# Kernel optimization log

Hardware: AMD Instinct MI355X
Metric: run time of the kernel (lower is better)

Reference implementation:

```python
import jax, jax.numpy as jnp
import numpy as np
import math

D_MODEL = 1024
MEM_SIZE = 4096
N_HEADS = 8
BATCH = 4
SEQ = 1024
TOP_K = min(SEQ, MEM_SIZE // 10)  # 409, matches torch: min(seq_len, memory_size//10)
UPDATE_RATE = 0.01


def _gelu(x):
    return jax.nn.gelu(x, approximate=False)  # torch nn.GELU default (erf)


def setup_inputs() -> dict:
    key = jax.random.key(0)
    ks = jax.random.split(key, 26)
    w = lambda k, shape, s=0.02: (jax.random.normal(k, shape, jnp.float32) * s)
    inp = {
        "x": jax.random.normal(ks[0], (BATCH, SEQ, D_MODEL), jnp.float32),
        "memory_bank": jax.random.normal(ks[1], (MEM_SIZE, D_MODEL), jnp.float32) * 0.1,
        "memory_indices": jax.random.randint(ks[2], (BATCH, TOP_K), 0, MEM_SIZE, jnp.int32),
        # memory_encoder: Linear -> GELU -> Linear
        "enc_w1": w(ks[3], (D_MODEL, D_MODEL)), "enc_b1": jnp.zeros((D_MODEL,), jnp.float32),
        "enc_w2": w(ks[4], (D_MODEL, D_MODEL)), "enc_b2": jnp.zeros((D_MODEL,), jnp.float32),
        # MultiheadAttention in/out projections
        "wq": w(ks[5], (D_MODEL, D_MODEL)), "bq": jnp.zeros((D_MODEL,), jnp.float32),
        "wk": w(ks[6], (D_MODEL, D_MODEL)), "bk": jnp.zeros((D_MODEL,), jnp.float32),
        "wv": w(ks[7], (D_MODEL, D_MODEL)), "bv": jnp.zeros((D_MODEL,), jnp.float32),
        "wo": w(ks[8], (D_MODEL, D_MODEL)), "bo": jnp.zeros((D_MODEL,), jnp.float32),
        # memory_decoder: Linear -> GELU -> Linear
        "dec_w1": w(ks[9], (D_MODEL, D_MODEL)), "dec_b1": jnp.zeros((D_MODEL,), jnp.float32),
        "dec_w2": w(ks[10], (D_MODEL, D_MODEL)), "dec_b2": jnp.zeros((D_MODEL,), jnp.float32),
        # LayerNorm
        "ln_g": jnp.ones((D_MODEL,), jnp.float32), "ln_b": jnp.zeros((D_MODEL,), jnp.float32),
        # importance_scorer: Linear(d,64) -> GELU -> Linear(64,1) -> Sigmoid
        "imp_w1": w(ks[11], (D_MODEL, 64)), "imp_b1": jnp.zeros((64,), jnp.float32),
        "imp_w2": w(ks[12], (64, 1)), "imp_b2": jnp.zeros((1,), jnp.float32),
    }
    return inp


def reference(x, memory_bank, memory_indices,
              enc_w1, enc_b1, enc_w2, enc_b2,
              wq, bq, wk, bk, wv, bv, wo, bo,
              dec_w1, dec_b1, dec_w2, dec_b2,
              ln_g, ln_b, imp_w1, imp_b1, imp_w2, imp_b2):
    B, L, D = x.shape
    M = memory_bank.shape[0]
    H = N_HEADS
    dh = D // H

    # memory_encoder (dropout inactive at eval)
    enc = _gelu(x @ enc_w1 + enc_b1) @ enc_w2 + enc_b2  # [B,L,D]

    # cross-attention: query = encoded input, key/value = memory bank (shared across batch)
    q = (enc @ wq + bq).reshape(B, L, H, dh)
    k = (memory_bank @ wk + bk).reshape(M, H, dh)
    v = (memory_bank @ wv + bv).reshape(M, H, dh)
    scores = jnp.einsum('blhd,mhd->bhlm', q, k) * (1.0 / math.sqrt(dh))
    attn = jax.nn.softmax(scores, axis=-1)                 # [B,H,L,M]
    ctx = jnp.einsum('bhlm,mhd->blhd', attn, v).reshape(B, L, D)
    mem_out = ctx @ wo + bo

    # memory_decoder + residual + LayerNorm
    dec = _gelu(mem_out @ dec_w1 + dec_b1) @ dec_w2 + dec_b2
    comb = x + dec
    mu = jnp.mean(comb, axis=-1, keepdims=True)
    var = jnp.var(comb, axis=-1, keepdims=True)
    out = (comb - mu) / jnp.sqrt(var + 1e-5) * ln_g + ln_b  # [B,L,D]

    # _update_memory: importance top-k select + sequential EMA scatter into memory bank
    imp = jax.nn.sigmoid(_gelu(x @ imp_w1 + imp_b1) @ imp_w2 + imp_b2)[..., 0]  # [B,L]
    _, top_idx = jax.lax.top_k(imp, TOP_K)                  # [B,K]
    top_tok = jnp.take_along_axis(x, top_idx[..., None], axis=1)  # [B,K,D]

    # faithful to the torch double loop (b outer, k inner): sequential EMA with
    # chained updates on index collisions
    flat_idx = memory_indices.reshape(-1)
    flat_tok = top_tok.reshape(-1, D)

    def body(mem, xs):
        i, t = xs
        row = (1.0 - UPDATE_RATE) * mem[i] + UPDATE_RATE * t
        return mem.at[i].set(row), None

    new_mem, _ = jax.lax.scan(body, memory_bank, (flat_idx, flat_tok))
    return out, new_mem
```

## Files before the change

### kernel.cpp

```cpp
#include <hip/hip_runtime.h>

typedef unsigned short u16;
typedef __attribute__((ext_vector_type(4))) int i4;
typedef __attribute__((ext_vector_type(4))) unsigned u4;
typedef __attribute__((ext_vector_type(4))) unsigned short us4;
typedef __attribute__((ext_vector_type(8))) short short8;
typedef __attribute__((ext_vector_type(4))) float f4;

#define D_MODEL 1024
#define ROWS 4096
#define NHEAD 8
#define DH 128
#define TOPK 409
#define NUPD 1636
#define NBATCH 4
#define MAXC 64
#define ATTNROWS 32768
#define QSCALE 0.1275174038f

__device__ __forceinline__ u16 f2bf(float f) {
  unsigned u = __builtin_bit_cast(unsigned, f);
  u += 0x7fffu + ((u >> 16) & 1u);
  return (u16)(u >> 16);
}
__device__ __forceinline__ float bf2f(u16 b) {
  unsigned u = ((unsigned)b) << 16;
  return __builtin_bit_cast(float, u);
}
__device__ __forceinline__ float ex2(float x) {
  return __builtin_amdgcn_exp2f(x);
}
__device__ __forceinline__ float gelu_f(float v) {
  return 0.5f * v * (1.0f + erff(v * 0.70710678118654752f));
}
__device__ __forceinline__ void gload16(const void* g, void* l) {
  __builtin_amdgcn_global_load_lds((const __attribute__((address_space(1))) void*)g,
                                   (__attribute__((address_space(3))) void*)l, 16, 0, 0);
}

__global__ __launch_bounds__(256) void conv2_kernel(const float* __restrict__ in0,
                                                    u16* __restrict__ out0,
                                                    const float* __restrict__ in1,
                                                    u16* __restrict__ out1, int nb) {
  int bid = blockIdx.x;
  const float* in = (bid < nb) ? in0 : in1;
  u16* out = (bid < nb) ? out0 : out1;
  int i = (bid < nb ? bid : bid - nb) * 256 + threadIdx.x;
  f4 v = ((const f4*)in)[i];
  us4 o;
  o.x = f2bf(v.x); o.y = f2bf(v.y); o.z = f2bf(v.z); o.w = f2bf(v.w);
  ((us4*)out)[i] = o;
}

__global__ __launch_bounds__(256) void wtrans8_kernel(const float* s0, const float* s1,
                                                      const float* s2, const float* s3,
                                                      const float* s4, const float* s5,
                                                      const float* s6, const float* s7,
                                                      u16* __restrict__ dst) {
  const float* srcs[8] = {s0, s1, s2, s3, s4, s5, s6, s7};
  const float* w = srcs[blockIdx.z];
  u16* wt = dst + (size_t)blockIdx.z * (1024 * 1024);
  __shared__ float t[32][33];
  int tx = threadIdx.x & 31, ty = threadIdx.x >> 5;
  int k0 = blockIdx.y * 32, n0 = blockIdx.x * 32;
  for (int r = 0; r < 4; ++r)
    t[ty + r * 8][tx] = w[(size_t)(k0 + ty + r * 8) * 1024 + n0 + tx];
  __syncthreads();
  for (int r = 0; r < 4; ++r)
    wt[(size_t)(n0 + ty + r * 8) * 1024 + k0 + tx] = f2bf(t[tx][ty + r * 8]);
}

__global__ __launch_bounds__(256) void bias_partB(const float* __restrict__ pbuf,
                                                  const float* __restrict__ bq,
                                                  const float* __restrict__ db1,
                                                  float* __restrict__ bqp,
                                                  float* __restrict__ bodp) {
  int id = blockIdx.x;
  int which = id >> 2;
  int n = (id & 3) * 256 + threadIdx.x;
  float s = 0.0f;
  for (int kb = 0; kb < 8; ++kb) s += pbuf[(size_t)(which * 8 + kb) * 1024 + n];
  float* out = which ? bodp : bqp;
  const float* badd = which ? db1 : bq;
  out[n] = s + badd[n];
}

__device__ __forceinline__ void gemm_core(const u16* __restrict__ A,
                                          const u16* __restrict__ BT,
                                          char* al, char* bl, int m0, int n0,
                                          f4 acc[4][2]) {
  const int K = 1024;
  const int tid = threadIdx.x;
  const int lane = tid & 63;
  const int g = lane >> 4, qi = lane & 15;
  const int wid = tid >> 6;
  const int wr = wid >> 1, wc = wid & 1;
  const int a0r = tid >> 2, a0b = (tid & 3) ^ ((a0r >> 1) & 3);
  const int c1 = tid + 256;
  const int a1r = c1 >> 2, a1b = (c1 & 3) ^ ((a1r >> 1) & 3);
  const int b0r = tid >> 2, b0b = (tid & 3) ^ ((b0r >> 1) & 3);

#define STAGE(buf, kt)                                                                   \
  {                                                                                      \
    const int k0_ = (kt) * 32;                                                           \
    gload16(A + (size_t)(m0 + a0r) * K + k0_ + a0b * 8, al + (buf) * 8192 + tid * 16);   \
    gload16(A + (size_t)(m0 + a1r) * K + k0_ + a1b * 8, al + (buf) * 8192 + c1 * 16);    \
    gload16(BT + (size_t)(n0 + b0r) * K + k0_ + b0b * 8, bl + (buf) * 4096 + tid * 16);  \
  }

  STAGE(0, 0);
  __syncthreads();
  int cur = 0;
  for (int kt = 0; kt < 32; ++kt) {
    if (kt + 1 < 32) STAGE(cur ^ 1, kt + 1);
    short8 af[4], bfr[2];
    for (int i = 0; i < 4; ++i) {
      int r = wr * 64 + i * 16 + qi;
      af[i] = *(const short8*)(al + cur * 8192 + r * 64 + ((g ^ ((r >> 1) & 3))) * 16);
    }
    for (int sn = 0; sn < 2; ++sn) {
      int r = wc * 32 + sn * 16 + qi;
      bfr[sn] = *(const short8*)(bl + cur * 4096 + r * 64 + ((g ^ ((r >> 1) & 3))) * 16);
    }
    for (int i = 0; i < 4; ++i)
      for (int sn = 0; sn < 2; ++sn)
        acc[i][sn] = __builtin_amdgcn_mfma_f32_16x16x32_bf16(af[i], bfr[sn], acc[i][sn], 0, 0, 0);
    __syncthreads();
    cur ^= 1;
  }
#undef STAGE
}

__global__ __launch_bounds__(256) void mega_kernel(
    const u16* __restrict__ Akv, const u16* __restrict__ BTkv,
    const float* __restrict__ bk, const float* __restrict__ bv,
    u16* __restrict__ Ck, u16* __restrict__ CvT,
    const u16* __restrict__ Ae, const u16* __restrict__ BTe,
    const float* __restrict__ be, u16* __restrict__ Ce,
    const u16* __restrict__ A0, const u16* __restrict__ B0, u16* __restrict__ C0,
    const u16* __restrict__ A1, const u16* __restrict__ B1, u16* __restrict__ C1,
    const float* __restrict__ b2, const float* __restrict__ wqf,
    const float* __restrict__ bo, const float* __restrict__ dw1,
    float* __restrict__ pbuf,
    const float* __restrict__ x, const float* __restrict__ iw1,
    const float* __restrict__ ib1, const float* __restrict__ iw2,
    const float* __restrict__ ib2, float* __restrict__ imp) {
  __shared__ __align__(16) char pool[32768];
  char* al = pool;
  char* bl = pool + 2 * 128 * 64;
  const int gid = blockIdx.x;
  const int tid = threadIdx.x;
  const int lane = tid & 63, wid = tid >> 6;
  const int g = lane >> 4, qi = lane & 15;
  const int wr = wid >> 1, wc = wid & 1;

  if (gid < 1024) {
    const int xcd = gid & 7, j = gid >> 3;
    const int m0 = ((j & 3) * 8 + xcd) * 128;
    const int n0 = (j >> 2) * 64;
    f4 acc[4][2] = {};
    gemm_core(Akv, BTkv, al, bl, m0, n0, acc);
    if (n0 < 1024) {
      for (int i = 0; i < 4; ++i) {
        int row = m0 + wr * 64 + i * 16 + g * 4;
        for (int sn = 0; sn < 2; ++sn) {
          int col = n0 + wc * 32 + sn * 16 + qi;
          float bvv = bk[col];
          for (int jj = 0; jj < 4; ++jj)
            Ck[(size_t)(row + jj) * 1024 + col] = f2bf(acc[i][sn][jj] + bvv);
        }
      }
    } else {
      u16(*t)[132] = (u16(*)[132])pool;
      __syncthreads();
      for (int i = 0; i < 4; ++i)
        for (int sn = 0; sn < 2; ++sn) {
          int nl = wc * 32 + sn * 16 + qi;
          float bvv = bv[n0 - 1024 + nl];
          for (int jj = 0; jj < 4; ++jj)
            t[nl][wr * 64 + i * 16 + g * 4 + jj] = f2bf(acc[i][sn][jj] + bvv);
        }
      __syncthreads();
      int r = tid >> 2, cg = tid & 3;
      for (int v = 0; v < 4; ++v) {
        us4 val = *(const us4*)&t[r][cg * 32 + v * 8];
        *(us4*)&CvT[(size_t)(n0 - 1024 + r) * 4096 + m0 + cg * 32 + v * 8] = val;
      }
    }
  } else if (gid < 1536) {
    const int id = gid - 1024;
    const int xcd = id & 7, j = id >> 3;
    const int m0 = ((j & 3) * 8 + xcd) * 128;
    const int n0 = (j >> 2) * 64;
    f4 acc[4][2] = {};
    gemm_core(Ae, BTe, al, bl, m0, n0, acc);
    for (int i = 0; i < 4; ++i) {
      int row = m0 + wr * 64 + i * 16 + g * 4;
      for (int sn = 0; sn < 2; ++sn) {
        int col = n0 + wc * 32 + sn * 16 + qi;
        float bv = be[col];
        for (int jj = 0; jj < 4; ++jj)
          Ce[(size_t)(row + jj) * 1024 + col] = f2bf(gelu_f(acc[i][sn][jj] + bv));
      }
    }
  } else if (gid < 1792) {
    const int id = gid - 1536;
    const int which = id >> 7, j = id & 127;
    const u16* A = which ? A1 : A0;
    const u16* BT = which ? B1 : B0;
    u16* C = which ? C1 : C0;
    const int m0 = (j >> 4) * 128, n0 = (j & 15) * 64;
    f4 acc[4][2] = {};
    gemm_core(A, BT, al, bl, m0, n0, acc);
    for (int i = 0; i < 4; ++i) {
      int row = m0 + wr * 64 + i * 16 + g * 4;
      for (int sn = 0; sn < 2; ++sn) {
        int col = n0 + wc * 32 + sn * 16 + qi;
        for (int jj = 0; jj < 4; ++jj)
          C[(size_t)(row + jj) * 1024 + col] = f2bf(acc[i][sn][jj]);
      }
    }
  } else if (gid < 1856) {
    const int lid = gid - 1792;
    const int which = lid >> 5;
    const int kb = (lid >> 2) & 7;
    const int n = (lid & 3) * 256 + tid;
    const float* bvec = which ? bo : b2;
    const float* W = which ? dw1 : wqf;
    float s = 0.0f;
    for (int k = kb * 128; k < kb * 128 + 128; ++k) s += bvec[k] * W[(size_t)k * 1024 + n];
    pbuf[(size_t)(which * 8 + kb) * 1024 + n] = s;
  } else {
    const int lid = gid - 1856;
    float* xs = (float*)pool;
    size_t base = (size_t)lid * 8192;
    for (int i = 0; i < 32; ++i) xs[tid + i * 256] = x[base + tid + i * 256];
    __syncthreads();
    int r0 = wid * 2, r1 = wid * 2 + 1;
    float a0 = 0.0f, a1 = 0.0f;
    for (int k = 0; k < 1024; ++k) {
      float wv = iw1[k * 64 + lane];
      a0 += xs[r0 * 1024 + k] * wv;
      a1 += xs[r1 * 1024 + k] * wv;
    }
    float h0 = gelu_f(a0 + ib1[lane]) * iw2[lane];
    float h1 = gelu_f(a1 + ib1[lane]) * iw2[lane];
    for (int d = 1; d < 64; d <<= 1) {
      h0 += __shfl_xor(h0, d, 64);
      h1 += __shfl_xor(h1, d, 64);
    }
    if (lane == 0) {
      imp[lid * 8 + r0] = 1.0f / (1.0f + expf(-(h0 + ib2[0])));
      imp[lid * 8 + r1] = 1.0f / (1.0f + expf(-(h1 + ib2[0])));
    }
  }
}

template <int EPI>
__global__ __launch_bounds__(256) void gemm_bt(const u16* __restrict__ A,
                                               const u16* __restrict__ BT,
                                               const float* __restrict__ bias,
                                               void* __restrict__ C) {
  __shared__ __align__(16) char al[2 * 128 * 64];
  __shared__ __align__(16) char bl[2 * 64 * 64];
  const int N = 1024;
  const int id = blockIdx.x;
  const int xcd = id & 7, j = id >> 3;
  const int m0 = ((j & 3) * 8 + xcd) * 128;
  const int n0 = (j >> 2) * 64;
  const int tid = threadIdx.x;
  const int lane = tid & 63, wid = tid >> 6;
  const int g = lane >> 4, qi = lane & 15;
  const int wr = wid >> 1, wc = wid & 1;
  f4 acc[4][2] = {};
  gemm_core(A, BT, al, bl, m0, n0, acc);
  for (int i = 0; i < 4; ++i) {
    int row = m0 + wr * 64 + i * 16 + g * 4;
    for (int sn = 0; sn < 2; ++sn) {
      int col = n0 + wc * 32 + sn * 16 + qi;
      float bv = bias[col];
      for (int jj = 0; jj < 4; ++jj) {
        float v = acc[i][sn][jj] + bv;
        if constexpr (EPI == 1) v = gelu_f(v);
        if constexpr (EPI == 4) v = v * QSCALE;
        if constexpr (EPI == 2)
          ((float*)C)[(size_t)(row + jj) * N + col] = v;
        else
          ((u16*)C)[(size_t)(row + jj) * N + col] = f2bf(v);
      }
    }
  }
}

template <int LP>
__global__ __launch_bounds__(512) void attn_kernel(const u16* __restrict__ q,
                                                   const u16* __restrict__ kp,
                                                   const u16* __restrict__ vT,
                                                   u16* __restrict__ cp0, u16* __restrict__ cp1,
                                                   u16* __restrict__ cp2, u16* __restrict__ cp3,
                                                   float* __restrict__ ml) {
  constexpr int MR = 4096 >> LP;
  constexpr int NT = MR / 64;
  __shared__ __align__(16) char kl[64 * 256];
  __shared__ __align__(16) char vl[128 * 128];
  const int id = blockIdx.x;
  const int h = id & 7;
  const int rest = id >> 3;
  const int part = rest & ((1 << LP) - 1);
  const int qblk = (rest >> LP) & 7;
  const int b = rest >> (3 + LP);
  const int tid = threadIdx.x;
  const int lane = tid & 63, wid = tid >> 6;
  const int g = lane >> 4, qi = lane & 15;
  const int qrow = b * 1024 + qblk * 128 + wid * 16 + qi;
  u16* ctp = (part == 0) ? cp0 : (part == 1) ? cp1 : (part == 2) ? cp2 : cp3;

  short8 qf[4];
  for (int kk = 0; kk < 4; ++kk)
    qf[kk] = *(const short8*)(q + (size_t)qrow * 1024 + h * 128 + kk * 32 + g * 8);

  const int kc0 = tid, kc1 = tid + 512;
  const int kr0 = kc0 >> 4, kb0 = kc0 & 15, kr1 = kc1 >> 4, kb1 = kc1 & 15;
  const int vr0 = kc0 >> 3, vb0 = kc0 & 7, vr1 = kc1 >> 3, vb1 = kc1 & 7;
  const int kd0 = kr0 * 256 + (kb0 ^ (kr0 & 7)) * 16;
  const int kd1 = kr1 * 256 + (kb1 ^ (kr1 & 7)) * 16;
  const int vd0 = vr0 * 128 + (vb0 ^ (vr0 & 7)) * 16;
  const int vd1 = vr1 * 128 + (vb1 ^ (vr1 & 7)) * 16;
  const int mbase = part * MR;
  const u16* kg0 = kp + (size_t)kr0 * 1024 + h * 128 + kb0 * 8;
  const u16* kg1 = kp + (size_t)kr1 * 1024 + h * 128 + kb1 * 8;
  const u16* vg0 = vT + (size_t)(h * 128 + vr0) * 4096 + vb0 * 8;
  const u16* vg1 = vT + (size_t)(h * 128 + vr1) * 4096 + vb1 * 8;

  i4 kreg0, kreg1, vreg0, vreg1;
#define LOADREGS(mt_)                                  \
  {                                                    \
    const int m0_ = mbase + (mt_) * 64;                \
    kreg0 = *(const i4*)(kg0 + (size_t)m0_ * 1024);    \
    kreg1 = *(const i4*)(kg1 + (size_t)m0_ * 1024);    \
    vreg0 = *(const i4*)(vg0 + m0_);                   \
    vreg1 = *(const i4*)(vg1 + m0_);                   \
  }

  f4 ct[8] = {};
  float mrun = -1e30f, lsum = 0.0f;

  LOADREGS(0);
  for (int mt = 0; mt < NT; ++mt) {
    __syncthreads();
    *(i4*)(kl + kd0) = kreg0;
    *(i4*)(kl + kd1) = kreg1;
    *(i4*)(vl + vd0) = vreg0;
    *(i4*)(vl + vd1) = vreg1;
    __syncthreads();
    if (mt + 1 < NT) LOADREGS(mt + 1);

    f4 st[4] = {};
    for (int s = 0; s < 4; ++s) {
      int n = s * 16 + qi;
      const char* krow = kl + n * 256;
      int sw = n & 7;
      for (int kk = 0; kk < 4; ++kk) {
        short8 a = *(const short8*)(krow + ((kk * 4 + g) ^ sw) * 16);
        st[s] = __builtin_amdgcn_mfma_f32_16x16x32_bf16(a, qf[kk], st[s], 0, 0, 0);
      }
    }
    float sv[16];
    float tm = -1e30f;
    for (int s = 0; s < 4; ++s)
      for (int jj = 0; jj < 4; ++jj) {
        sv[s * 4 + jj] = st[s][jj];
        tm = fmaxf(tm, st[s][jj]);
      }
    tm = fmaxf(tm, __shfl_xor(tm, 16, 64));
    tm = fmaxf(tm, __shfl_xor(tm, 32, 64));
    if (!__all(tm <= mrun + 8.0f)) {
      float mnew = fmaxf(mrun, tm);
      float r = ex2(mrun - mnew);
      lsum *= r;
      for (int i = 0; i < 8; ++i) ct[i] = ct[i] * r;
      mrun = mnew;
    }
    float psum = 0.0f;
    for (int i = 0; i < 16; ++i) {
      float p = ex2(sv[i] - mrun);
      sv[i] = p;
      psum += p;
    }
    psum += __shfl_xor(psum, 16, 64);
    psum += __shfl_xor(psum, 32, 64);
    lsum += psum;

    unsigned pk0[4], pk1[4];
    for (int s = 0; s < 4; ++s) {
      pk0[s] = (unsigned)f2bf(sv[s * 4 + 0]) | ((unsigned)f2bf(sv[s * 4 + 1]) << 16);
      pk1[s] = (unsigned)f2bf(sv[s * 4 + 2]) | ((unsigned)f2bf(sv[s * 4 + 3]) << 16);
    }
    const int src1 = qi + ((g & 1) << 5);
    const int src2 = src1 + 16;
    const bool hi = (g & 2) != 0;
    for (int p = 0; p < 2; ++p) {
      unsigned a0 = __shfl(pk0[2 * p], src1, 64), b0 = __shfl(pk0[2 * p + 1], src1, 64);
      unsigned a1 = __shfl(pk1[2 * p], src1, 64), b1 = __shfl(pk1[2 * p + 1], src1, 64);
      unsigned a2 = __shfl(pk0[2 * p], src2, 64), b2 = __shfl(pk0[2 * p + 1], src2, 64);
      unsigned a3 = __shfl(pk1[2 * p], src2, 64), b3 = __shfl(pk1[2 * p + 1], src2, 64);
      u4 bw;
      bw.x = hi ? b0 : a0; bw.y = hi ? b1 : a1; bw.z = hi ? b2 : a2; bw.w = hi ? b3 : a3;
      short8 pf = __builtin_bit_cast(short8, bw);
      for (int d = 0; d < 8; ++d) {
        int dr = d * 16 + qi;
        short8 a = *(const short8*)(vl + dr * 128 + (((p * 4 + g) ^ (dr & 7))) * 16);
        ct[d] = __builtin_amdgcn_mfma_f32_16x16x32_bf16(a, pf, ct[d], 0, 0, 0);
      }
    }
  }
#undef LOADREGS

  const int orow = ((b * 8 + h) << 10) + qblk * 128 + wid * 16 + qi;
  if (g == 0) {
    ml[(size_t)(part * ATTNROWS + orow) * 2 + 0] = mrun;
    ml[(size_t)(part * ATTNROWS + orow) * 2 + 1] = lsum;
  }
  for (int d = 0; d < 8; ++d) {
    us4 o;
    o.x = f2bf(ct[d][0]); o.y = f2bf(ct[d][1]);
    o.z = f2bf(ct[d][2]); o.w = f2bf(ct[d][3]);
    *(us4*)(ctp + (size_t)orow * 128 + d * 16 + g * 4) = o;
  }
}

__global__ __launch_bounds__(256) void combine4_kernel(const u16* __restrict__ cp0,
                                                       const u16* __restrict__ cp1,
                                                       const u16* __restrict__ cp2,
                                                       const u16* __restrict__ cp3,
                                                       const float* __restrict__ ml,
                                                       u16* __restrict__ ctx) {
  int tid = threadIdx.x;
  int row = blockIdx.x * 16 + (tid >> 4);
  int dp = (tid & 15) * 8;
  float m0 = ml[(size_t)row * 2], l0 = ml[(size_t)row * 2 + 1];
  float m1 = ml[((size_t)ATTNROWS + row) * 2], l1 = ml[((size_t)ATTNROWS + row) * 2 + 1];
  float m2 = ml[((size_t)2 * ATTNROWS + row) * 2], l2 = ml[((size_t)2 * ATTNROWS + row) * 2 + 1];
  float m3 = ml[((size_t)3 * ATTNROWS + row) * 2], l3 = ml[((size_t)3 * ATTNROWS + row) * 2 + 1];
  float m = fmaxf(fmaxf(m0, m1), fmaxf(m2, m3));
  float s0 = ex2(m0 - m), s1 = ex2(m1 - m), s2 = ex2(m2 - m), s3 = ex2(m3 - m);
  float inv = 1.0f / (l0 * s0 + l1 * s1 + l2 * s2 + l3 * s3);
  short8 c0 = *(const short8*)(cp0 + (size_t)row * 128 + dp);
  short8 c1 = *(const short8*)(cp1 + (size_t)row * 128 + dp);
  short8 c2 = *(const short8*)(cp2 + (size_t)row * 128 + dp);
  short8 c3 = *(const short8*)(cp3 + (size_t)row * 128 + dp);
  us4 o[2];
  for (int i = 0; i < 8; ++i) {
    float f = (bf2f((u16)c0[i]) * s0 + bf2f((u16)c1[i]) * s1 + bf2f((u16)c2[i]) * s2 +
               bf2f((u16)c3[i]) * s3) * inv;
    ((u16*)o)[i] = f2bf(f);
  }
  int bb = row >> 13, hh = (row >> 10) & 7, qr = row & 1023;
  *(short8*)(ctx + (size_t)((bb << 10) + qr) * 1024 + hh * 128 + dp) =
      __builtin_bit_cast(short8, o);
}

__global__ __launch_bounds__(256) void ln_kernel(const float* __restrict__ x,
                                                 const float* __restrict__ dec,
                                                 const float* __restrict__ gw,
                                                 const float* __restrict__ bw,
                                                 float* __restrict__ out,
                                                 int* __restrict__ cnt) {
  __shared__ float rs[256], rs2[256];
  int row = blockIdx.x, tid = threadIdx.x;
  if (tid == 0) cnt[row] = 0;
  float c[4];
  float s = 0.0f, s2 = 0.0f;
  for (int i = 0; i < 4; ++i) {
    int col = tid + i * 256;
    float v = x[(size_t)row * 1024 + col] + dec[(size_t)row * 1024 + col];
    c[i] = v; s += v; s2 += v * v;
  }
  rs[tid] = s; rs2[tid] = s2;
  __syncthreads();
  for (int st = 128; st > 0; st >>= 1) {
    if (tid < st) { rs[tid] += rs[tid + st]; rs2[tid] += rs2[tid + st]; }
    __syncthreads();
  }
  float mu = rs[0] * (1.0f / 1024.0f);
  float var = rs2[0] * (1.0f / 1024.0f) - mu * mu;
  float inv = rsqrtf(var + 1e-5f);
  for (int i = 0; i < 4; ++i) {
    int col = tid + i * 256;
    out[(size_t)row * 1024 + col] = (c[i] - mu) * inv * gw[col] + bw[col];
  }
}

__global__ __launch_bounds__(512) void topk_kernel(const float* __restrict__ imp,
                                                   int* __restrict__ tidx) {
  __shared__ float v[1024];
  __shared__ int ix[1024];
  int b = blockIdx.x, tid = threadIdx.x;
  for (int i = tid; i < 1024; i += 512) { v[i] = imp[b * 1024 + i]; ix[i] = i; }
  __syncthreads();
  for (int k = 2; k <= 1024; k <<= 1) {
    for (int j = k >> 1; j > 0; j >>= 1) {
      for (int t = tid; t < 1024; t += 512) {
        int p = t ^ j;
        if (p > t) {
          float va = v[t], vb = v[p];
          int ia = ix[t], ib = ix[p];
          bool ord = (va > vb) || (va == vb && ia < ib);
          bool up = ((t & k) == 0);
          if (up ? !ord : ord) { v[t] = vb; v[p] = va; ix[t] = ib; ix[p] = ia; }
        }
      }
      __syncthreads();
    }
  }
  for (int t = tid; t < TOPK; t += 512) tidx[b * TOPK + t] = ix[t];
}

__global__ __launch_bounds__(128) void rank_kernel(const int* __restrict__ midx,
                                                   int* __restrict__ cnt,
                                                   int* __restrict__ slot) {
  __shared__ int mi[NUPD];
  int tid = threadIdx.x;
  for (int i = tid; i < NUPD; i += 128) mi[i] = midx[i];
  __syncthreads();
  int j = blockIdx.x * 128 + tid;
  if (j < NUPD) {
    int r = mi[j], rank = 0;
    for (int jp = 0; jp < j; ++jp) rank += (mi[jp] == r) ? 1 : 0;
    if (rank < MAXC) slot[r * MAXC + rank] = j;
    atomicAdd(&cnt[r], 1);
  }
}

__global__ __launch_bounds__(256) void apply_kernel(const float* __restrict__ x,
                                                    const float* __restrict__ mem,
                                                    const int* __restrict__ tidx,
                                                    const int* __restrict__ cnt,
                                                    const int* __restrict__ slot,
                                                    float* __restrict__ outm) {
  int row = blockIdx.x, tid = threadIdx.x;
  f4 acc = ((const f4*)(mem + (size_t)row * 1024))[tid];
  int c = cnt[row];
  c = c < MAXC ? c : MAXC;
  for (int t = 0; t < c; ++t) {
    int j = slot[row * MAXC + t];
    int b = j / TOPK;
    int tr = tidx[j];
    f4 xv = ((const f4*)(x + ((size_t)b * 1024 + tr) * 1024))[tid];
    acc = acc * 0.99f + xv * 0.01f;
  }
  ((f4*)(outm + (size_t)row * 1024))[tid] = acc;
}

extern "C" void kernel_launch(void* const* d_in, const int* in_sizes, int n_in,
                              void* d_out, int out_size, void* d_ws, size_t ws_size,
                              hipStream_t stream) {
  const float* x = (const float*)d_in[0];
  const float* memory_bank = (const float*)d_in[1];
  const int* memory_indices = (const int*)d_in[2];
  const float* enc_w1 = (const float*)d_in[3];
  const float* enc_b1 = (const float*)d_in[4];
  const float* enc_w2 = (const float*)d_in[5];
  const float* enc_b2 = (const float*)d_in[6];
  const float* wq = (const float*)d_in[7];
  const float* bq = (const float*)d_in[8];
  const float* wk = (const float*)d_in[9];
  const float* bk = (const float*)d_in[10];
  const float* wv = (const float*)d_in[11];
  const float* bv = (const float*)d_in[12];
  const float* wo = (const float*)d_in[13];
  const float* bo = (const float*)d_in[14];
  const float* dec_w1 = (const float*)d_in[15];
  const float* dec_b1 = (const float*)d_in[16];
  const float* dec_w2 = (const float*)d_in[17];
  const float* dec_b2 = (const float*)d_in[18];
  const float* ln_g = (const float*)d_in[19];
  const float* ln_b = (const float*)d_in[20];
  const float* imp_w1 = (const float*)d_in[21];
  const float* imp_b1 = (const float*)d_in[22];
  const float* imp_w2 = (const float*)d_in[23];
  const float* imp_b2 = (const float*)d_in[24];

  char* ws = (char*)d_ws;
  u16* buf0 = (u16*)(ws);
  u16* buf1 = (u16*)(ws + (8ull << 20));
  u16* buf2 = (u16*)(ws + (16ull << 20));
  u16* buf3 = (u16*)(ws + (24ull << 20));
  u16* buf4 = (u16*)(ws + (32ull << 20));
  float* decb = (float*)(ws + (40ull << 20));
  u16* wtb = (u16*)(ws + (56ull << 20));
  float* impb = (float*)(ws + (72ull << 20));
  int* tidx = (int*)(ws + (72ull << 20) + (1 << 16));
  float* bqp = (float*)(ws + (72ull << 20) + (1 << 17));
  float* bodp = (float*)(ws + (72ull << 20) + (1 << 17) + 4096);
  float* pbuf = (float*)(ws + (72ull << 20) + 196608);
  int* cnt = (int*)buf3;
  int* slot = (int*)(ws + (24ull << 20) + (1 << 16));
  u16* w2n = (u16*)(ws + (40ull << 20));
  u16* won = (u16*)(ws + (42ull << 20));
  u16* cp0 = buf1;
  u16* cp1 = buf2;
  u16* cp2 = (u16*)(ws + (40ull << 20));
  u16* cp3 = (u16*)(ws + (48ull << 20));
  float* ml = (float*)(ws + (56ull << 20));

  const int NM = 1024 * 1024;
  u16* wt_e1 = wtb + 0 * NM;
  u16* wt_e2q = wtb + 1 * NM;
  u16* wt_q = wtb + 2 * NM;
  u16* wt_k = wtb + 3 * NM;
  u16* wt_od = wtb + 5 * NM;
  u16* wt_d1 = wtb + 6 * NM;
  u16* wt_d2 = wtb + 7 * NM;

  conv2_kernel<<<8192, 256, 0, stream>>>(x, buf0, memory_bank, buf2, 4096);
  wtrans8_kernel<<<dim3(32, 32, 8), 256, 0, stream>>>(enc_w1, enc_w2, wq, wk, wv, wo,
                                                      dec_w1, dec_w2, wtb);
  conv2_kernel<<<2048, 256, 0, stream>>>(enc_w2, w2n, wo, won, 1024);

  mega_kernel<<<2368, 256, 0, stream>>>(buf2, wt_k, bk, bv, buf3, buf4,
                                        buf0, wt_e1, enc_b1, buf1,
                                        wt_q, w2n, wt_e2q, wt_d1, won, wt_od,
                                        enc_b2, wq, bo, dec_w1, pbuf,
                                        x, imp_w1, imp_b1, imp_w2, imp_b2, impb);
  bias_partB<<<8, 256, 0, stream>>>(pbuf, bq, dec_b1, bqp, bodp);

  gemm_bt<4><<<512, 256, 0, stream>>>(buf1, wt_e2q, bqp, buf0);

  attn_kernel<2><<<1024, 512, 0, stream>>>(buf0, buf3, buf4, cp0, cp1, cp2, cp3, ml);
  combine4_kernel<<<2048, 256, 0, stream>>>(cp0, cp1, cp2, cp3, ml, buf0);

  gemm_bt<1><<<512, 256, 0, stream>>>(buf0, wt_od, bodp, buf1);
  gemm_bt<2><<<512, 256, 0, stream>>>(buf1, wt_d2, dec_b2, decb);
  ln_kernel<<<4096, 256, 0, stream>>>(x, decb, ln_g, ln_b, (float*)d_out, cnt);

  topk_kernel<<<NBATCH, 512, 0, stream>>>(impb, tidx);
  rank_kernel<<<13, 128, 0, stream>>>(memory_indices, cnt, slot);
  apply_kernel<<<4096, 256, 0, stream>>>(x, memory_bank, tidx, cnt, slot,
                                         (float*)d_out + (size_t)ROWS * D_MODEL);
}
```

Baseline: 391.5 us.

## Process two query tiles per wave and halve the KV split in attention

Each wave in the attention kernel now handles 32 query rows, two 16-row tiles, so every K and V fragment loaded from shared memory feeds two MFMAs. The memory dimension is split into 2 partitions instead of 4, which shrinks the partial outputs and the combine step to two inputs. The grid falls from 1024 to 256 blocks of 512 threads, which may leave many compute units idle on a large GPU. Doubling the accumulators also raises register pressure.

```diff
diff --git a/kernel.cpp b/kernel.cpp
--- a/kernel.cpp
+++ b/kernel.cpp
@@ -297,7 +297,6 @@
                                                    const u16* __restrict__ kp,
                                                    const u16* __restrict__ vT,
                                                    u16* __restrict__ cp0, u16* __restrict__ cp1,
-                                                   u16* __restrict__ cp2, u16* __restrict__ cp3,
                                                    float* __restrict__ ml) {
   constexpr int MR = 4096 >> LP;
   constexpr int NT = MR / 64;
@@ -307,132 +306,159 @@
   const int h = id & 7;
   const int rest = id >> 3;
   const int part = rest & ((1 << LP) - 1);
-  const int qblk = (rest >> LP) & 7;
-  const int b = rest >> (3 + LP);
+  const int qsec = (rest >> LP) & 3;
+  const int b = rest >> (2 + LP);
   const int tid = threadIdx.x;
   const int lane = tid & 63, wid = tid >> 6;
   const int g = lane >> 4, qi = lane & 15;
-  const int qrow = b * 1024 + qblk * 128 + wid * 16 + qi;
-  u16* ctp = (part == 0) ? cp0 : (part == 1) ? cp1 : (part == 2) ? cp2 : cp3;
-
-  short8 qf[4];
-  for (int kk = 0; kk < 4; ++kk)
-    qf[kk] = *(const short8*)(q + (size_t)qrow * 1024 + h * 128 + kk * 32 + g * 8);
-
-  const int kc0 = tid, kc1 = tid + 512;
-  const int kr0 = kc0 >> 4, kb0 = kc0 & 15, kr1 = kc1 >> 4, kb1 = kc1 & 15;
-  const int vr0 = kc0 >> 3, vb0 = kc0 & 7, vr1 = kc1 >> 3, vb1 = kc1 & 7;
+  const int qrow0 = b * 1024 + qsec * 256 + wid * 32 + qi;
+  const int qrow1 = qrow0 + 16;
+  u16* ctp = (part == 0) ? cp0 : cp1;
+
+  short8 qf0[4], qf1[4];
+  for (int kk = 0; kk < 4; ++kk) {
+    qf0[kk] = *(const short8*)(q + (size_t)qrow0 * 1024 + h * 128 + kk * 32 + g * 8);
+    qf1[kk] = *(const short8*)(q + (size_t)qrow1 * 1024 + h * 128 + kk * 32 + g * 8);
+  }
+
+  const int kc1 = tid + 512;
+  const int kr0 = tid >> 4, kb0 = tid & 15, kr1 = kc1 >> 4, kb1 = kc1 & 15;
+  const int vr0 = tid >> 3, vb0 = tid & 7, vr1 = kc1 >> 3, vb1 = kc1 & 7;
   const int kd0 = kr0 * 256 + (kb0 ^ (kr0 & 7)) * 16;
   const int kd1 = kr1 * 256 + (kb1 ^ (kr1 & 7)) * 16;
   const int vd0 = vr0 * 128 + (vb0 ^ (vr0 & 7)) * 16;
   const int vd1 = vr1 * 128 + (vb1 ^ (vr1 & 7)) * 16;
   const int mbase = part * MR;
-  const u16* kg0 = kp + (size_t)kr0 * 1024 + h * 128 + kb0 * 8;
-  const u16* kg1 = kp + (size_t)kr1 * 1024 + h * 128 + kb1 * 8;
-  const u16* vg0 = vT + (size_t)(h * 128 + vr0) * 4096 + vb0 * 8;
-  const u16* vg1 = vT + (size_t)(h * 128 + vr1) * 4096 + vb1 * 8;
+  const u16* kg0 = kp + (size_t)(mbase + kr0) * 1024 + h * 128 + kb0 * 8;
+  const u16* kg1 = kp + (size_t)(mbase + kr1) * 1024 + h * 128 + kb1 * 8;
+  const u16* vg0 = vT + (size_t)(h * 128 + vr0) * 4096 + mbase + vb0 * 8;
+  const u16* vg1 = vT + (size_t)(h * 128 + vr1) * 4096 + mbase + vb1 * 8;
 
   i4 kreg0, kreg1, vreg0, vreg1;
-#define LOADREGS(mt_)                                  \
-  {                                                    \
-    const int m0_ = mbase + (mt_) * 64;                \
-    kreg0 = *(const i4*)(kg0 + (size_t)m0_ * 1024);    \
-    kreg1 = *(const i4*)(kg1 + (size_t)m0_ * 1024);    \
-    vreg0 = *(const i4*)(vg0 + m0_);                   \
-    vreg1 = *(const i4*)(vg1 + m0_);                   \
-  }
-
-  f4 ct[8] = {};
-  float mrun = -1e30f, lsum = 0.0f;
-
-  LOADREGS(0);
+#define LOADREGS()                              \
+  {                                             \
+    kreg0 = *(const i4*)kg0; kg0 += 64 * 1024;  \
+    kreg1 = *(const i4*)kg1; kg1 += 64 * 1024;  \
+    vreg0 = *(const i4*)vg0; vg0 += 64;         \
+    vreg1 = *(const i4*)vg1; vg1 += 64;         \
+  }
+
+  f4 ct0[8] = {}, ct1[8] = {};
+  float mrun0 = -1e30f, lsum0 = 0.0f, mrun1 = -1e30f, lsum1 = 0.0f;
+
+  LOADREGS();
   for (int mt = 0; mt < NT; ++mt) {
     __syncthreads();
-    *(i4*)(kl + kd0) = kreg0;
-    *(i4*)(kl + kd1) = kreg1;
-    *(i4*)(vl + vd0) = vreg0;
-    *(i4*)(vl + vd1) = vreg1;
+    *(i4*)(kl + kd0) = kreg0; *(i4*)(kl + kd1) = kreg1;
+    *(i4*)(vl + vd0) = vreg0; *(i4*)(vl + vd1) = vreg1;
     __syncthreads();
-    if (mt + 1 < NT) LOADREGS(mt + 1);
-
-    f4 st[4] = {};
+    if (mt + 1 < NT) LOADREGS();
+
+    f4 st0[4] = {}, st1[4] = {};
     for (int s = 0; s < 4; ++s) {
       int n = s * 16 + qi;
       const char* krow = kl + n * 256;
       int sw = n & 7;
       for (int kk = 0; kk < 4; ++kk) {
         short8 a = *(const short8*)(krow + ((kk * 4 + g) ^ sw) * 16);
-        st[s] = __builtin_amdgcn_mfma_f32_16x16x32_bf16(a, qf[kk], st[s], 0, 0, 0);
+        st0[s] = __builtin_amdgcn_mfma_f32_16x16x32_bf16(a, qf0[kk], st0[s], 0, 0, 0);
+        st1[s] = __builtin_amdgcn_mfma_f32_16x16x32_bf16(a, qf1[kk], st1[s], 0, 0, 0);
       }
     }
-    float sv[16];
-    float tm = -1e30f;
-    for (int s = 0; s < 4; ++s)
-      for (int jj = 0; jj < 4; ++jj) {
-        sv[s * 4 + jj] = st[s][jj];
-        tm = fmaxf(tm, st[s][jj]);
-      }
-    tm = fmaxf(tm, __shfl_xor(tm, 16, 64));
-    tm = fmaxf(tm, __shfl_xor(tm, 32, 64));
-    if (!__all(tm <= mrun + 8.0f)) {
-      float mnew = fmaxf(mrun, tm);
-      float r = ex2(mrun - mnew);
-      lsum *= r;
-      for (int i = 0; i < 8; ++i) ct[i] = ct[i] * r;
-      mrun = mnew;
-    }
-    float psum = 0.0f;
-    for (int i = 0; i < 16; ++i) {
-      float p = ex2(sv[i] - mrun);
-      sv[i] = p;
-      psum += p;
-    }
-    psum += __shfl_xor(psum, 16, 64);
-    psum += __shfl_xor(psum, 32, 64);
-    lsum += psum;
-
-    unsigned pk0[4], pk1[4];
-    for (int s = 0; s < 4; ++s) {
-      pk0[s] = (unsigned)f2bf(sv[s * 4 + 0]) | ((unsigned)f2bf(sv[s * 4 + 1]) << 16);
-      pk1[s] = (unsigned)f2bf(sv[s * 4 + 2]) | ((unsigned)f2bf(sv[s * 4 + 3]) << 16);
-    }
-    const int src1 = qi + ((g & 1) << 5);
-    const int src2 = src1 + 16;
-    const bool hi = (g & 2) != 0;
-    for (int p = 0; p < 2; ++p) {
-      unsigned a0 = __shfl(pk0[2 * p], src1, 64), b0 = __shfl(pk0[2 * p + 1], src1, 64);
-      unsigned a1 = __shfl(pk1[2 * p], src1, 64), b1 = __shfl(pk1[2 * p + 1], src1, 64);
-      unsigned a2 = __shfl(pk0[2 * p], src2, 64), b2 = __shfl(pk0[2 * p + 1], src2, 64);
-      unsigned a3 = __shfl(pk1[2 * p], src2, 64), b3 = __shfl(pk1[2 * p + 1], src2, 64);
-      u4 bw;
-      bw.x = hi ? b0 : a0; bw.y = hi ? b1 : a1; bw.z = hi ? b2 : a2; bw.w = hi ? b3 : a3;
-      short8 pf = __builtin_bit_cast(short8, bw);
-      for (int d = 0; d < 8; ++d) {
-        int dr = d * 16 + qi;
-        short8 a = *(const short8*)(vl + dr * 128 + (((p * 4 + g) ^ (dr & 7))) * 16);
-        ct[d] = __builtin_amdgcn_mfma_f32_16x16x32_bf16(a, pf, ct[d], 0, 0, 0);
-      }
+
+    short8 pfa0, pfb0, pfa1, pfb1;
+#define SOFTMAX_PACK(ST, MRUN, LSUM, CT, PFA, PFB)                                        \
+    {                                                                                     \
+      float sv[16];                                                                       \
+      float tm = -1e30f;                                                                  \
+      for (int s = 0; s < 4; ++s)                                                         \
+        for (int jj = 0; jj < 4; ++jj) {                                                  \
+          sv[s * 4 + jj] = ST[s][jj];                                                     \
+          tm = fmaxf(tm, ST[s][jj]);                                                      \
+        }                                                                                 \
+      tm = fmaxf(tm, __shfl_xor(tm, 16, 64));                                             \
+      tm = fmaxf(tm, __shfl_xor(tm, 32, 64));                                             \
+      if (!__all(tm <= MRUN + 8.0f)) {                                                    \
+        float mnew = fmaxf(MRUN, tm);                                                     \
+        float r = ex2(MRUN - mnew);                                                       \
+        LSUM *= r;                                                                        \
+        for (int i = 0; i < 8; ++i) CT[i] = CT[i] * r;                                    \
+        MRUN = mnew;                                                                      \
+      }                                                                                   \
+      float psum = 0.0f;                                                                  \
+      for (int i = 0; i < 16; ++i) {                                                      \
+        float p = ex2(sv[i] - MRUN);                                                      \
+        sv[i] = p;                                                                        \
+        psum += p;                                                                        \
+      }                                                                                   \
+      psum += __shfl_xor(psum, 16, 64);                                                   \
+      psum += __shfl_xor(psum, 32, 64);                                                   \
+      LSUM += psum;                                                                       \
+      unsigned pk0[4], pk1[4];                                                            \
+      for (int s = 0; s < 4; ++s) {                                                       \
+        pk0[s] = (unsigned)f2bf(sv[s * 4 + 0]) | ((unsigned)f2bf(sv[s * 4 + 1]) << 16);   \
+        pk1[s] = (unsigned)f2bf(sv[s * 4 + 2]) | ((unsigned)f2bf(sv[s * 4 + 3]) << 16);   \
+      }                                                                                   \
+      const int src1 = qi + ((g & 1) << 5);                                               \
+      const int src2 = src1 + 16;                                                         \
+      const bool hi = (g & 2) != 0;                                                       \
+      {                                                                                   \
+        unsigned a0 = __shfl(pk0[0], src1, 64), b0 = __shfl(pk0[1], src1, 64);            \
+        unsigned a1 = __shfl(pk1[0], src1, 64), b1 = __shfl(pk1[1], src1, 64);            \
+        unsigned a2 = __shfl(pk0[0], src2, 64), b2 = __shfl(pk0[1], src2, 64);            \
+        unsigned a3 = __shfl(pk1[0], src2, 64), b3 = __shfl(pk1[1], src2, 64);            \
+        u4 bw;                                                                            \
+        bw.x = hi ? b0 : a0; bw.y = hi ? b1 : a1; bw.z = hi ? b2 : a2; bw.w = hi ? b3 : a3;\
+        PFA = __builtin_bit_cast(short8, bw);                                             \
+      }                                                                                   \
+      {                                                                                   \
+        unsigned a0 = __shfl(pk0[2], src1, 64), b0 = __shfl(pk0[3], src1, 64);            \
+        unsigned a1 = __shfl(pk1[2], src1, 64), b1 = __shfl(pk1[3], src1, 64);            \
+        unsigned a2 = __shfl(pk0[2], src2, 64), b2 = __shfl(pk0[3], src2, 64);            \
+        unsigned a3 = __shfl(pk1[2], src2, 64), b3 = __shfl(pk1[3], src2, 64);            \
+        u4 bw;                                                                            \
+        bw.x = hi ? b0 : a0; bw.y = hi ? b1 : a1; bw.z = hi ? b2 : a2; bw.w = hi ? b3 : a3;\
+        PFB = __builtin_bit_cast(short8, bw);                                             \
+      }                                                                                   \
+    }
+    SOFTMAX_PACK(st0, mrun0, lsum0, ct0, pfa0, pfb0);
+    SOFTMAX_PACK(st1, mrun1, lsum1, ct1, pfa1, pfb1);
+#undef SOFTMAX_PACK
+
+    for (int d = 0; d < 8; ++d) {
+      int dr = d * 16 + qi;
+      const char* vrow = vl + dr * 128;
+      int swv = dr & 7;
+      short8 a0 = *(const short8*)(vrow + ((0 + g) ^ swv) * 16);
+      ct0[d] = __builtin_amdgcn_mfma_f32_16x16x32_bf16(a0, pfa0, ct0[d], 0, 0, 0);
+      ct1[d] = __builtin_amdgcn_mfma_f32_16x16x32_bf16(a0, pfa1, ct1[d], 0, 0, 0);
+      short8 a1 = *(const short8*)(vrow + ((4 + g) ^ swv) * 16);
+      ct0[d] = __builtin_amdgcn_mfma_f32_16x16x32_bf16(a1, pfb0, ct0[d], 0, 0, 0);
+      ct1[d] = __builtin_amdgcn_mfma_f32_16x16x32_bf16(a1, pfb1, ct1[d], 0, 0, 0);
     }
   }
 #undef LOADREGS
 
-  const int orow = ((b * 8 + h) << 10) + qblk * 128 + wid * 16 + qi;
+  const int obase = ((b * 8 + h) << 10) + qsec * 256 + wid * 32 + qi;
   if (g == 0) {
-    ml[(size_t)(part * ATTNROWS + orow) * 2 + 0] = mrun;
-    ml[(size_t)(part * ATTNROWS + orow) * 2 + 1] = lsum;
+    ml[(size_t)(part * ATTNROWS + obase) * 2 + 0] = mrun0;
+    ml[(size_t)(part * ATTNROWS + obase) * 2 + 1] = lsum0;
+    ml[(size_t)(part * ATTNROWS + obase + 16) * 2 + 0] = mrun1;
+    ml[(size_t)(part * ATTNROWS + obase + 16) * 2 + 1] = lsum1;
   }
   for (int d = 0; d < 8; ++d) {
-    us4 o;
-    o.x = f2bf(ct[d][0]); o.y = f2bf(ct[d][1]);
-    o.z = f2bf(ct[d][2]); o.w = f2bf(ct[d][3]);
-    *(us4*)(ctp + (size_t)orow * 128 + d * 16 + g * 4) = o;
-  }
-}
-
-__global__ __launch_bounds__(256) void combine4_kernel(const u16* __restrict__ cp0,
+    us4 o0, o1;
+    o0.x = f2bf(ct0[d][0]); o0.y = f2bf(ct0[d][1]);
+    o0.z = f2bf(ct0[d][2]); o0.w = f2bf(ct0[d][3]);
+    o1.x = f2bf(ct1[d][0]); o1.y = f2bf(ct1[d][1]);
+    o1.z = f2bf(ct1[d][2]); o1.w = f2bf(ct1[d][3]);
+    *(us4*)(ctp + (size_t)obase * 128 + d * 16 + g * 4) = o0;
+    *(us4*)(ctp + (size_t)(obase + 16) * 128 + d * 16 + g * 4) = o1;
+  }
+}
+
+__global__ __launch_bounds__(256) void combine2_kernel(const u16* __restrict__ cp0,
                                                        const u16* __restrict__ cp1,
-                                                       const u16* __restrict__ cp2,
-                                                       const u16* __restrict__ cp3,
                                                        const float* __restrict__ ml,
                                                        u16* __restrict__ ctx) {
   int tid = threadIdx.x;
@@ -440,19 +466,14 @@
   int dp = (tid & 15) * 8;
   float m0 = ml[(size_t)row * 2], l0 = ml[(size_t)row * 2 + 1];
   float m1 = ml[((size_t)ATTNROWS + row) * 2], l1 = ml[((size_t)ATTNROWS + row) * 2 + 1];
-  float m2 = ml[((size_t)2 * ATTNROWS + row) * 2], l2 = ml[((size_t)2 * ATTNROWS + row) * 2 + 1];
-  float m3 = ml[((size_t)3 * ATTNROWS + row) * 2], l3 = ml[((size_t)3 * ATTNROWS + row) * 2 + 1];
-  float m = fmaxf(fmaxf(m0, m1), fmaxf(m2, m3));
-  float s0 = ex2(m0 - m), s1 = ex2(m1 - m), s2 = ex2(m2 - m), s3 = ex2(m3 - m);
-  float inv = 1.0f / (l0 * s0 + l1 * s1 + l2 * s2 + l3 * s3);
+  float m = fmaxf(m0, m1);
+  float s0 = ex2(m0 - m), s1 = ex2(m1 - m);
+  float inv = 1.0f / (l0 * s0 + l1 * s1);
   short8 c0 = *(const short8*)(cp0 + (size_t)row * 128 + dp);
   short8 c1 = *(const short8*)(cp1 + (size_t)row * 128 + dp);
-  short8 c2 = *(const short8*)(cp2 + (size_t)row * 128 + dp);
-  short8 c3 = *(const short8*)(cp3 + (size_t)row * 128 + dp);
   us4 o[2];
   for (int i = 0; i < 8; ++i) {
-    float f = (bf2f((u16)c0[i]) * s0 + bf2f((u16)c1[i]) * s1 + bf2f((u16)c2[i]) * s2 +
-               bf2f((u16)c3[i]) * s3) * inv;
+    float f = (bf2f((u16)c0[i]) * s0 + bf2f((u16)c1[i]) * s1) * inv;
     ((u16*)o)[i] = f2bf(f);
   }
   int bb = row >> 13, hh = (row >> 10) & 7, qr = row & 1023;
@@ -600,8 +621,6 @@
   u16* won = (u16*)(ws + (42ull << 20));
   u16* cp0 = buf1;
   u16* cp1 = buf2;
-  u16* cp2 = (u16*)(ws + (40ull << 20));
-  u16* cp3 = (u16*)(ws + (48ull << 20));
   float* ml = (float*)(ws + (56ull << 20));
 
   const int NM = 1024 * 1024;
@@ -627,8 +646,8 @@
 
   gemm_bt<4><<<512, 256, 0, stream>>>(buf1, wt_e2q, bqp, buf0);
 
-  attn_kernel<2><<<1024, 512, 0, stream>>>(buf0, buf3, buf4, cp0, cp1, cp2, cp3, ml);
-  combine4_kernel<<<2048, 256, 0, stream>>>(cp0, cp1, cp2, cp3, ml, buf0);
+  attn_kernel<1><<<256, 512, 0, stream>>>(buf0, buf3, buf4, cp0, cp1, ml);
+  combine2_kernel<<<2048, 256, 0, stream>>>(cp0, cp1, ml, buf0);
 
   gemm_bt<1><<<512, 256, 0, stream>>>(buf0, wt_od, bodp, buf1);
   gemm_bt<2><<<512, 256, 0, stream>>>(buf1, wt_d2, dec_b2, decb);
```

New measurement: 374.8 us (median of 3 runs). 1.04x faster.
